# Optimization experiments

Hardware: AMD Instinct MI355X
Metric: run time of the kernel (lower is better)

The kernel has to match this reference:

```python
import jax, jax.numpy as jnp
import numpy as np

EMB = 256
N_HEADS = 8
N_LVLS = 4
N_POINTS = 4
HEAD_DIM = EMB // N_HEADS  # 32
D_FFN = 1024
SHAPES = [(100, 100), (50, 50), (25, 25), (13, 13)]
LEN = sum(h * w for h, w in SHAPES)  # 13294
B = 4


def setup_inputs() -> dict:
    key = jax.random.key(0)
    ks = jax.random.split(key, 20)
    rn = lambda k, s, sc=0.02: jax.random.normal(k, s, jnp.float32) * sc
    starts = np.cumsum([0] + [h * w for h, w in SHAPES])[:-1]
    return {
        'features': jax.random.normal(ks[0], (B, LEN, EMB), jnp.float32),
        'pos': jax.random.normal(ks[1], (B, LEN, EMB), jnp.float32),
        'reference_points': jax.random.uniform(ks[2], (B, LEN, N_LVLS, 2), jnp.float32),
        'spatial_shapes': jnp.array(SHAPES, jnp.int32),
        'lvl_start_idx': jnp.array(starts, jnp.int32),
        'W_off': rn(ks[3], (EMB, N_HEADS * N_LVLS * N_POINTS * 2)),
        'b_off': rn(ks[4], (N_HEADS * N_LVLS * N_POINTS * 2,), 0.5),
        'W_attn': rn(ks[5], (EMB, N_HEADS * N_LVLS * N_POINTS)),
        'b_attn': rn(ks[6], (N_HEADS * N_LVLS * N_POINTS,)),
        'W_val': rn(ks[7], (EMB, EMB)),
        'b_val': rn(ks[8], (EMB,)),
        'W_out': rn(ks[9], (EMB, EMB)),
        'b_out': rn(ks[10], (EMB,)),
        'ln1_g': jnp.ones((EMB,), jnp.float32),
        'ln1_b': jnp.zeros((EMB,), jnp.float32),
        'W1': rn(ks[11], (EMB, D_FFN)),
        'b1': rn(ks[12], (D_FFN,)),
        'W2': rn(ks[13], (D_FFN, EMB)),
        'b2': rn(ks[14], (EMB,)),
        'ln2_g': jnp.ones((EMB,), jnp.float32),
        'ln2_b': jnp.zeros((EMB,), jnp.float32),
    }


def _layer_norm(x, g, b, eps=1e-5):
    mu = jnp.mean(x, axis=-1, keepdims=True)
    var = jnp.mean(jnp.square(x - mu), axis=-1, keepdims=True)
    return (x - mu) * jax.lax.rsqrt(var + eps) * g + b


def _ms_deform_attn(q, features, reference_points, shapes, starts,
                    W_off, b_off, W_attn, b_attn, W_val, b_val, W_out, b_out):
    Bn, Lq, D = features.shape
    value = (features @ W_val + b_val).reshape(Bn, Lq, N_HEADS, HEAD_DIM)
    off = (q @ W_off + b_off).reshape(Bn, Lq, N_HEADS, N_LVLS, N_POINTS, 2)
    attn = (q @ W_attn + b_attn).reshape(Bn, Lq, N_HEADS, N_LVLS * N_POINTS)
    attn = jax.nn.softmax(attn, axis=-1).reshape(Bn, Lq, N_HEADS, N_LVLS, N_POINTS)
    # normalizer per level is (W, H) for (x, y)
    norm = jnp.array([[w, h] for h, w in shapes], jnp.float32)  # (L, 2)
    loc = reference_points[:, :, None, :, None, :] + off / norm[None, None, None, :, None, :]

    out = jnp.zeros((Bn, N_HEADS, Lq, HEAD_DIM), value.dtype)
    for l, (H_, W_) in enumerate(shapes):
        s = starts[l]
        val = value[:, s:s + H_ * W_].transpose(0, 2, 1, 3)  # (B, nH, HW, Dh)
        locl = loc[:, :, :, l]  # (B, Lq, nH, P, 2), in [0,1]
        # grid_sample align_corners=False convention
        x = locl[..., 0] * W_ - 0.5
        y = locl[..., 1] * H_ - 0.5
        x0 = jnp.floor(x); y0 = jnp.floor(y)
        wx = x - x0; wy = y - y0
        x0i = x0.astype(jnp.int32); y0i = y0.astype(jnp.int32)

        def corner(xi, yi, w):
            valid = (xi >= 0) & (xi < W_) & (yi >= 0) & (yi < H_)
            idx = jnp.clip(yi, 0, H_ - 1) * W_ + jnp.clip(xi, 0, W_ - 1)  # (B, Lq, nH, P)
            idx = idx.transpose(0, 2, 1, 3).reshape(Bn, N_HEADS, Lq * N_POINTS, 1)
            g = jnp.take_along_axis(val, idx, axis=2)  # (B, nH, Lq*P, Dh)
            wm = (w * valid.astype(w.dtype)).transpose(0, 2, 1, 3).reshape(Bn, N_HEADS, Lq * N_POINTS, 1)
            return g * wm

        samp = (corner(x0i, y0i, (1 - wx) * (1 - wy))
                + corner(x0i + 1, y0i, wx * (1 - wy))
                + corner(x0i, y0i + 1, (1 - wx) * wy)
                + corner(x0i + 1, y0i + 1, wx * wy))
        samp = samp.reshape(Bn, N_HEADS, Lq, N_POINTS, HEAD_DIM)
        aw = attn[:, :, :, l].transpose(0, 2, 1, 3)  # (B, nH, Lq, P)
        out = out + jnp.einsum('bhqpd,bhqp->bhqd', samp, aw)

    out = out.transpose(0, 2, 1, 3).reshape(Bn, Lq, D)
    return out @ W_out + b_out


def reference(features, pos, reference_points, spatial_shapes, lvl_start_idx,
              W_off, b_off, W_attn, b_attn, W_val, b_val, W_out, b_out,
              ln1_g, ln1_b, W1, b1, W2, b2, ln2_g, ln2_b):
    shapes = [tuple(int(v) for v in r) for r in np.asarray(spatial_shapes)]
    starts = [int(v) for v in np.asarray(lvl_start_idx)]
    q = features + pos
    attn_out = _ms_deform_attn(q, features, reference_points, shapes, starts,
                               W_off, b_off, W_attn, b_attn, W_val, b_val, W_out, b_out)
    x = _layer_norm(features + attn_out, ln1_g, ln1_b)  # dropout is identity in eval
    ffn = jax.nn.relu(x @ W1 + b1) @ W2 + b2
    x = _layer_norm(x + ffn, ln2_g, ln2_b)  # stochastic depth is identity in eval
    return x
```

## Files before the change

kernel.cpp:

```cpp
#include <hip/hip_runtime.h>
#include <stdint.h>

#define LEN_T 13294
#define M_TOK 53176

typedef unsigned short u16;
typedef __bf16 bf16x8 __attribute__((ext_vector_type(8)));
typedef float f32x4 __attribute__((ext_vector_type(4)));
typedef float f32x2 __attribute__((ext_vector_type(2)));
typedef uint32_t u32x4 __attribute__((ext_vector_type(4)));
typedef uint32_t u32x2 __attribute__((ext_vector_type(2)));

__device__ __forceinline__ u16 f2bf(float f) {
    union { float f; uint32_t u; } v; v.f = f;
    uint32_t r = v.u + 0x7fffu + ((v.u >> 16) & 1u);
    return (u16)(r >> 16);
}
__device__ __forceinline__ float bf2f(u16 s) {
    union { uint32_t u; float f; } v; v.u = ((uint32_t)s) << 16;
    return v.f;
}
__device__ __forceinline__ u16 f2h(float f) {
    union { _Float16 h; u16 u; } c; c.h = (_Float16)f; return c.u;
}
__device__ __forceinline__ float hlo(uint32_t u) {
    union { uint32_t u; _Float16 h[2]; } v; v.u = u; return (float)v.h[0];
}
__device__ __forceinline__ float hhi(uint32_t u) {
    union { uint32_t u; _Float16 h[2]; } v; v.u = u; return (float)v.h[1];
}

__device__ __forceinline__ void gload_lds16(const u16* g, u16* l) {
    __builtin_amdgcn_global_load_lds(
        (const __attribute__((address_space(1))) uint32_t*)(g),
        (__attribute__((address_space(3))) uint32_t*)(l), 16, 0, 0);
}

__global__ __launch_bounds__(256) void prep_qf(
    const float* __restrict__ feat, const float* __restrict__ pos,
    u16* __restrict__ qb, u16* __restrict__ fb, int n4)
{
    int i = blockIdx.x * blockDim.x + threadIdx.x;
    int stride = gridDim.x * blockDim.x;
    for (; i < n4; i += stride) {
        float4 f = ((const float4*)feat)[i];
        float4 p = ((const float4*)pos)[i];
        uint32_t q0 = (uint32_t)f2bf(f.x + p.x) | ((uint32_t)f2bf(f.y + p.y) << 16);
        uint32_t q1 = (uint32_t)f2bf(f.z + p.z) | ((uint32_t)f2bf(f.w + p.w) << 16);
        uint32_t f0 = (uint32_t)f2bf(f.x) | ((uint32_t)f2bf(f.y) << 16);
        uint32_t f1 = (uint32_t)f2bf(f.z) | ((uint32_t)f2bf(f.w) << 16);
        ((uint2*)qb)[i] = make_uint2(q0, q1);
        ((uint2*)fb)[i] = make_uint2(f0, f1);
    }
}

__global__ __launch_bounds__(256) void wtrans_all(
    const float* __restrict__ W_val, const float* __restrict__ W_off,
    const float* __restrict__ W_attn, const float* __restrict__ W_out,
    const float* __restrict__ W1, const float* __restrict__ W2,
    u16* __restrict__ Wt_val, u16* __restrict__ Wt_oa,
    u16* __restrict__ Wt_out, u16* __restrict__ W1f, u16* __restrict__ W2f)
{
    int gid = blockIdx.x * 256 + threadIdx.x;
    if (gid < 229376) {
        const float* W; u16* D; int K, N, off;
        if      (gid < 65536)  { W = W_val;  D = Wt_val;        K = 256; N = 256; off = gid; }
        else if (gid < 131072) { W = W_off;  D = Wt_oa;         K = 256; N = 256; off = gid - 65536; }
        else if (gid < 163840) { W = W_attn; D = Wt_oa + 65536; K = 256; N = 128; off = gid - 131072; }
        else                   { W = W_out;  D = Wt_out;        K = 256; N = 256; off = gid - 163840; }
        int n = off / K, k = off - n * K;
        D[off] = f2bf(W[(size_t)k * N + n]);
    } else if (gid < 491520) {
        int off = gid - 229376;
        int e = off & 7, lane = (off >> 3) & 63;
        int r = off >> 9;
        int ks = r & 7, ni = (r >> 3) & 1, c = r >> 4;
        int col = c * 32 + ni * 16 + (lane & 15);
        int k = ks * 32 + (lane >> 4) * 8 + e;
        W1f[off] = f2bf(W1[(size_t)k * 1024 + col]);
    } else if (gid < 753664) {
        int off = gid - 491520;
        int e = off & 7, lane = (off >> 3) & 63;
        int r = off >> 9;
        int col = (r & 15) * 16 + (lane & 15);
        int k = (r >> 4) * 32 + (lane >> 4) * 8 + e;
        W2f[off] = f2bf(W2[(size_t)k * 256 + col]);
    }
}

#define MODE_VAL 0
#define MODE_OFFATTN 1

template<int MODE>
__global__ __launch_bounds__(256, 3) void gemm128(
    const u16* __restrict__ A, const u16* __restrict__ Bt,
    int M, int K,
    const float* __restrict__ bias, const float* __restrict__ bias2,
    void* __restrict__ out0, void* __restrict__ out1)
{
    __shared__ u16 Al[128 * 64];
    __shared__ u16 Bl[128 * 64];
    const int tid = threadIdx.x;
    const int lane = tid & 63;
    const int w = tid >> 6;
    const int wr = w >> 1, wc = w & 1;
    const int m0 = blockIdx.x * 128;
    const int n0 = blockIdx.y * 128;
    const int l15 = lane & 15;
    const int kg = lane >> 4;
    const int srow = lane >> 3;
    const int scol = (lane & 7) * 8;

    f32x4 acc[4][4];
#pragma unroll
    for (int i = 0; i < 4; ++i)
#pragma unroll
        for (int j = 0; j < 4; ++j)
            acc[i][j] = (f32x4){0.f, 0.f, 0.f, 0.f};

    const int nk = K >> 6;
    for (int kc = 0; kc < nk; ++kc) {
        __syncthreads();
#pragma unroll
        for (int j = 0; j < 4; ++j) {
            int c = w * 4 + j;
            int arow = m0 + c * 8 + srow;
            arow = arow < M ? arow : M - 1;
            gload_lds16(A + (size_t)arow * K + (kc << 6) + scol, Al + c * 512);
            int brow = n0 + c * 8 + srow;
            gload_lds16(Bt + (size_t)brow * K + (kc << 6) + scol, Bl + c * 512);
        }
        __syncthreads();
#pragma unroll
        for (int ks = 0; ks < 2; ++ks) {
            bf16x8 af[4], bfr[4];
#pragma unroll
            for (int i = 0; i < 4; ++i) {
                af[i]  = *(const bf16x8*)(Al + (wr * 64 + i * 16 + l15) * 64 + ks * 32 + kg * 8);
                bfr[i] = *(const bf16x8*)(Bl + (wc * 64 + i * 16 + l15) * 64 + ks * 32 + kg * 8);
            }
#pragma unroll
            for (int mi = 0; mi < 4; ++mi)
#pragma unroll
                for (int ni = 0; ni < 4; ++ni)
                    acc[mi][ni] = __builtin_amdgcn_mfma_f32_16x16x32_bf16(
                        af[mi], bfr[ni], acc[mi][ni], 0, 0, 0);
        }
    }

#pragma unroll
    for (int mi = 0; mi < 4; ++mi) {
#pragma unroll
        for (int r = 0; r < 4; ++r) {
            int row = m0 + wr * 64 + mi * 16 + kg * 4 + r;
            if (row >= M) continue;
#pragma unroll
            for (int ni = 0; ni < 4; ++ni) {
                int col = n0 + wc * 64 + ni * 16 + l15;
                float v = acc[mi][ni][r];
                if (MODE == MODE_VAL) {
                    int bI = row / LEN_T;
                    int t = row - bI * LEN_T;
                    int hh = col >> 5, d = col & 31;
                    ((u16*)out0)[((size_t)(bI * 8 + hh) * LEN_T + t) * 32 + d] =
                        f2h(v + bias[col]);
                } else {
                    if (col < 256) {
                        ((u16*)out0)[((size_t)(col >> 5) * M_TOK + row) * 32 + (col & 31)] =
                            f2h(v + bias[col]);
                    } else {
                        int c = col - 256;
                        ((u16*)out1)[((size_t)(c >> 4) * M_TOK + row) * 16 + (c & 15)] =
                            f2h(v + bias2[c]);
                    }
                }
            }
        }
    }
}

template<int KSTEPS, int OUTF32>
__global__ __launch_bounds__(256, 3) void gemm_ln(
    const u16* __restrict__ A, const u16* __restrict__ Bt,
    const float* __restrict__ bias, const u16* __restrict__ res,
    const float* __restrict__ g, const float* __restrict__ bb,
    u16* __restrict__ outb, float* __restrict__ outf, int M)
{
    __shared__ char ldsraw[40960];
    u16* Al = (u16*)ldsraw;
    u16* Bl = (u16*)(ldsraw + 8192);
    u16* dumpb = (u16*)ldsraw;
    const int tid = threadIdx.x;
    const int lane = tid & 63;
    const int w = tid >> 6;
    const int l15 = lane & 15;
    const int kg = lane >> 4;
    const int srow = lane >> 3;
    const int scol = (lane & 7) * 8;
    const int m0 = blockIdx.x * 64;
    const int K = KSTEPS * 64;

    f32x4 acc[4][4];
#pragma unroll
    for (int i = 0; i < 4; ++i)
#pragma unroll
        for (int j = 0; j < 4; ++j)
            acc[i][j] = (f32x4){0.f, 0.f, 0.f, 0.f};

    for (int kc = 0; kc < KSTEPS; ++kc) {
        __syncthreads();
#pragma unroll
        for (int j = 0; j < 2; ++j) {
            int c = w * 2 + j;
            int arow = m0 + c * 8 + srow;
            arow = arow < M ? arow : M - 1;
            gload_lds16(A + (size_t)arow * K + (kc << 6) + scol, Al + c * 512);
        }
#pragma unroll
        for (int j = 0; j < 8; ++j) {
            int c = w * 8 + j;
            int brow = c * 8 + srow;
            gload_lds16(Bt + (size_t)brow * K + (kc << 6) + scol, Bl + c * 512);
        }
        __syncthreads();
#pragma unroll
        for (int ks = 0; ks < 2; ++ks) {
            bf16x8 af[4], bfr[4];
#pragma unroll
            for (int i = 0; i < 4; ++i) {
                af[i]  = *(const bf16x8*)(Al + (i * 16 + l15) * 64 + ks * 32 + kg * 8);
                bfr[i] = *(const bf16x8*)(Bl + (w * 64 + i * 16 + l15) * 64 + ks * 32 + kg * 8);
            }
#pragma unroll
            for (int mi = 0; mi < 4; ++mi)
#pragma unroll
                for (int ni = 0; ni < 4; ++ni)
                    acc[mi][ni] = __builtin_amdgcn_mfma_f32_16x16x32_bf16(
                        af[mi], bfr[ni], acc[mi][ni], 0, 0, 0);
        }
    }

    __syncthreads();
#pragma unroll
    for (int mi = 0; mi < 4; ++mi) {
#pragma unroll
        for (int r = 0; r < 4; ++r) {
            int rr = mi * 16 + kg * 4 + r;
            int gr = m0 + rr; gr = gr < M ? gr : M - 1;
#pragma unroll
            for (int ni = 0; ni < 4; ++ni) {
                int col = w * 64 + ni * 16 + l15;
                dumpb[rr * 264 + col] = f2bf(acc[mi][ni][r] + bias[col] +
                                             bf2f(res[(size_t)gr * 256 + col]));
            }
        }
    }
    __syncthreads();

    float4 gv = *(const float4*)(g + lane * 4);
    float4 bv = *(const float4*)(bb + lane * 4);
#pragma unroll
    for (int i = 0; i < 16; ++i) {
        int rr = w * 16 + i;
        uint2 raw = *(const uint2*)(dumpb + rr * 264 + lane * 4);
        float x0 = bf2f((u16)(raw.x & 0xffff)), x1 = bf2f((u16)(raw.x >> 16));
        float x2 = bf2f((u16)(raw.y & 0xffff)), x3 = bf2f((u16)(raw.y >> 16));
        float s1 = x0 + x1 + x2 + x3;
        float s2 = x0*x0 + x1*x1 + x2*x2 + x3*x3;
#pragma unroll
        for (int o = 1; o < 64; o <<= 1) {
            s1 += __shfl_xor(s1, o);
            s2 += __shfl_xor(s2, o);
        }
        float mu = s1 * (1.0f / 256.0f);
        float var = s2 * (1.0f / 256.0f) - mu * mu;
        float rs = rsqrtf(var + 1e-5f);
        float o0 = (x0 - mu) * rs * gv.x + bv.x;
        float o1 = (x1 - mu) * rs * gv.y + bv.y;
        float o2 = (x2 - mu) * rs * gv.z + bv.z;
        float o3 = (x3 - mu) * rs * gv.w + bv.w;
        int grow = m0 + rr;
        if (grow < M) {
            if (OUTF32) {
                *(float4*)(outf + (size_t)grow * 256 + lane * 4) =
                    make_float4(o0, o1, o2, o3);
            } else {
                uint32_t u0 = (uint32_t)f2bf(o0) | ((uint32_t)f2bf(o1) << 16);
                uint32_t u1 = (uint32_t)f2bf(o2) | ((uint32_t)f2bf(o3) << 16);
                *(uint2*)(outb + (size_t)grow * 256 + lane * 4) = make_uint2(u0, u1);
            }
        }
    }
}

__global__ __launch_bounds__(256, 3) void ffn_fused(
    const u16* __restrict__ A, const u16* __restrict__ W1f, const u16* __restrict__ W2f,
    const float* __restrict__ b1, const float* __restrict__ b2,
    const float* __restrict__ g, const float* __restrict__ bb,
    float* __restrict__ outf, int M)
{
    __shared__ char lds[51200];
    u16* Axl = (u16*)lds;
    u16* ht  = (u16*)(lds + 33792);
    u16* dumpb = (u16*)lds;
    const int tid = threadIdx.x;
    const int lane = tid & 63;
    const int w = tid >> 6;
    const int l15 = lane & 15;
    const int kg = lane >> 4;
    const int m0 = blockIdx.x * 64;

#pragma unroll
    for (int i = 0; i < 8; ++i) {
        int linear = i * 256 + tid;
        int row = linear >> 5;
        int gcol = (linear & 31) * 8;
        int grow = m0 + row; grow = grow < M ? grow : M - 1;
        uint4 v = *(const uint4*)(A + (size_t)grow * 256 + gcol);
        *(uint4*)(Axl + row * 264 + gcol) = v;
    }
    __syncthreads();

    f32x4 acc[4][4];
#pragma unroll
    for (int i = 0; i < 4; ++i)
#pragma unroll
        for (int j = 0; j < 4; ++j)
            acc[i][j] = (f32x4){0.f, 0.f, 0.f, 0.f};
    f32x4 acc2[4][2];

#define ZERO_ACC2() \
    _Pragma("unroll") for (int i = 0; i < 4; ++i) { \
        acc2[i][0] = (f32x4){0.f,0.f,0.f,0.f}; acc2[i][1] = (f32x4){0.f,0.f,0.f,0.f}; }

#define FFN1_CHUNK(HC) { \
    _Pragma("unroll") for (int ks = 0; ks < 8; ++ks) { \
        bf16x8 af[4], bw[2]; \
        _Pragma("unroll") for (int ni = 0; ni < 2; ++ni) \
            bw[ni] = *(const bf16x8*)(W1f + ((size_t)(((((HC) * 4 + w) * 2 + ni) * 8 + ks)) << 9) + lane * 8); \
        _Pragma("unroll") for (int mi = 0; mi < 4; ++mi) \
            af[mi] = *(const bf16x8*)(Axl + (mi * 16 + l15) * 264 + ks * 32 + kg * 8); \
        _Pragma("unroll") for (int mi = 0; mi < 4; ++mi) \
            _Pragma("unroll") for (int ni = 0; ni < 2; ++ni) \
                acc2[mi][ni] = __builtin_amdgcn_mfma_f32_16x16x32_bf16(af[mi], bw[ni], acc2[mi][ni], 0, 0, 0); \
    } }

#define FFN2_CHUNK(HC) { \
    _Pragma("unroll") for (int ks2 = 0; ks2 < 4; ++ks2) { \
        bf16x8 ah[4], bw2[4]; \
        _Pragma("unroll") for (int ni = 0; ni < 4; ++ni) \
            bw2[ni] = *(const bf16x8*)(W2f + ((size_t)((((HC) * 4 + ks2) * 16 + w * 4 + ni)) << 9) + lane * 8); \
        _Pragma("unroll") for (int mi = 0; mi < 4; ++mi) \
            ah[mi] = *(const bf16x8*)(ht + (mi * 16 + l15) * 136 + ks2 * 32 + kg * 8); \
        _Pragma("unroll") for (int mi = 0; mi < 4; ++mi) \
            _Pragma("unroll") for (int ni = 0; ni < 4; ++ni) \
                acc[mi][ni] = __builtin_amdgcn_mfma_f32_16x16x32_bf16(ah[mi], bw2[ni], acc[mi][ni], 0, 0, 0); \
    } }

#define HT_WRITE(HC) { \
    _Pragma("unroll") for (int mi = 0; mi < 4; ++mi) \
        _Pragma("unroll") for (int ni = 0; ni < 2; ++ni) \
            _Pragma("unroll") for (int r = 0; r < 4; ++r) { \
                int rr = mi * 16 + kg * 4 + r; \
                int cl = w * 32 + ni * 16 + l15; \
                float hv = acc2[mi][ni][r] + b1[(HC) * 128 + cl]; \
                ht[rr * 136 + cl] = f2bf(hv > 0.f ? hv : 0.f); \
            } }

    ZERO_ACC2();
    FFN1_CHUNK(0);
    for (int hc = 0; hc < 8; ++hc) {
        __syncthreads();
        HT_WRITE(hc);
        __syncthreads();
        FFN2_CHUNK(hc);
        if (hc < 7) { ZERO_ACC2(); FFN1_CHUNK(hc + 1); }
    }

#pragma unroll
    for (int mi = 0; mi < 4; ++mi) {
#pragma unroll
        for (int r = 0; r < 4; ++r) {
            int rr = mi * 16 + kg * 4 + r;
#pragma unroll
            for (int ni = 0; ni < 4; ++ni) {
                int col = w * 64 + ni * 16 + l15;
                float v = acc[mi][ni][r] + b2[col] + bf2f(Axl[rr * 264 + col]);
                dumpb[rr * 264 + col] = f2bf(v);
            }
        }
    }
    __syncthreads();

    float4 gv = *(const float4*)(g + lane * 4);
    float4 bv = *(const float4*)(bb + lane * 4);
#pragma unroll
    for (int i = 0; i < 16; ++i) {
        int rr = w * 16 + i;
        uint2 raw = *(const uint2*)(dumpb + rr * 264 + lane * 4);
        float x0 = bf2f((u16)(raw.x & 0xffff)), x1 = bf2f((u16)(raw.x >> 16));
        float x2 = bf2f((u16)(raw.y & 0xffff)), x3 = bf2f((u16)(raw.y >> 16));
        float s1 = x0 + x1 + x2 + x3;
        float s2 = x0*x0 + x1*x1 + x2*x2 + x3*x3;
#pragma unroll
        for (int o = 1; o < 64; o <<= 1) {
            s1 += __shfl_xor(s1, o);
            s2 += __shfl_xor(s2, o);
        }
        float mu = s1 * (1.0f / 256.0f);
        float var = s2 * (1.0f / 256.0f) - mu * mu;
        float rs = rsqrtf(var + 1e-5f);
        float o0 = (x0 - mu) * rs * gv.x + bv.x;
        float o1 = (x1 - mu) * rs * gv.y + bv.y;
        float o2 = (x2 - mu) * rs * gv.z + bv.z;
        float o3 = (x3 - mu) * rs * gv.w + bv.w;
        int grow = m0 + rr;
        if (grow < M) {
            *(float4*)(outf + (size_t)grow * 256 + lane * 4) =
                make_float4(o0, o1, o2, o3);
        }
    }
}

__device__ __forceinline__ void acc8h(u32x4 v, float w, float* acc) {
    acc[0] = fmaf(hlo(v.x), w, acc[0]);
    acc[1] = fmaf(hhi(v.x), w, acc[1]);
    acc[2] = fmaf(hlo(v.y), w, acc[2]);
    acc[3] = fmaf(hhi(v.y), w, acc[3]);
    acc[4] = fmaf(hlo(v.z), w, acc[4]);
    acc[5] = fmaf(hhi(v.z), w, acc[5]);
    acc[6] = fmaf(hlo(v.w), w, acc[6]);
    acc[7] = fmaf(hhi(v.w), w, acc[7]);
}

__global__ __launch_bounds__(256, 4) void sample_kernel(
    const u16* __restrict__ offt, const u16* __restrict__ attnt,
    const u16* __restrict__ value, const float* __restrict__ refp,
    u16* __restrict__ samp)
{
    int bid = blockIdx.x;
    int lb  = (bid & 7) * 832 + (bid >> 3);
    int bh  = lb / 208;
    int tblk = lb - bh * 208;
    int pr  = threadIdx.x >> 2;
    int dq  = threadIdx.x & 3;
    int tok = tblk * 64 + pr;
    if (tok >= LEN_T) return;
    int b = bh >> 3, h = bh & 7;
    int lane = threadIdx.x & 63;
    size_t row = (size_t)b * LEN_T + tok;

    int W_    = dq == 0 ? 100 : dq == 1 ? 50 : dq == 2 ? 25 : 13;
    float Wf   = dq == 0 ? 100.f : dq == 1 ? 50.f : dq == 2 ? 25.f : 13.f;
    float invW = dq == 0 ? 0.01f : dq == 1 ? 0.02f : dq == 2 ? 0.04f : (1.0f / 13.0f);

    u32x2 av = __builtin_nontemporal_load(
        (const u32x2*)(attnt + ((size_t)h * M_TOK + row) * 16 + dq * 4));
    float e0 = hlo(av.x), e1 = hhi(av.x), e2 = hlo(av.y), e3 = hhi(av.y);
    float m = fmaxf(fmaxf(e0, e1), fmaxf(e2, e3));
    m = fmaxf(m, __shfl_xor(m, 1));
    m = fmaxf(m, __shfl_xor(m, 2));
    e0 = __expf(e0 - m); e1 = __expf(e1 - m);
    e2 = __expf(e2 - m); e3 = __expf(e3 - m);
    float s = e0 + e1 + e2 + e3;
    s += __shfl_xor(s, 1);
    s += __shfl_xor(s, 2);
    float inv = 1.0f / s;
    float awp[4] = {e0 * inv, e1 * inv, e2 * inv, e3 * inv};

    f32x2 rv = __builtin_nontemporal_load((const f32x2*)(refp + row * 8 + dq * 2));
    float rx = rv.x, ry = rv.y;
    u32x4 ov = __builtin_nontemporal_load(
        (const u32x4*)(offt + ((size_t)h * M_TOK + row) * 32 + dq * 8));
    float dxs[4] = {hlo(ov.x), hlo(ov.y), hlo(ov.z), hlo(ov.w)};
    float dys[4] = {hhi(ov.x), hhi(ov.y), hhi(ov.z), hhi(ov.w)};

    float wts[16]; int offs[16];
#pragma unroll
    for (int p = 0; p < 4; ++p) {
        float x = fmaf(fmaf(dxs[p], invW, rx), Wf, -0.5f);
        float y = fmaf(fmaf(dys[p], invW, ry), Wf, -0.5f);
        float x0f = floorf(x), y0f = floorf(y);
        int x0 = (int)x0f, y0 = (int)y0f;
        int x1 = x0 + 1, y1 = y0 + 1;
        float wx = x - x0f, wy = y - y0f;
        float vx0 = ((unsigned)x0 < (unsigned)W_) ? 1.f : 0.f;
        float vx1 = ((unsigned)x1 < (unsigned)W_) ? 1.f : 0.f;
        float vy0 = ((unsigned)y0 < (unsigned)W_) ? 1.f : 0.f;
        float vy1 = ((unsigned)y1 < (unsigned)W_) ? 1.f : 0.f;
        int cx0 = min(max(x0, 0), W_ - 1);
        int cx1 = min(max(x1, 0), W_ - 1);
        int cy0 = min(max(y0, 0), W_ - 1);
        int cy1 = min(max(y1, 0), W_ - 1);
        float a = awp[p];
        wts[p*4+0] = (1.f - wx) * (1.f - wy) * a * vx0 * vy0;
        wts[p*4+1] = wx * (1.f - wy) * a * vx1 * vy0;
        wts[p*4+2] = (1.f - wx) * wy * a * vx0 * vy1;
        wts[p*4+3] = wx * wy * a * vx1 * vy1;
        offs[p*4+0] = (cy0 * W_ + cx0) * 32;
        offs[p*4+1] = (cy0 * W_ + cx1) * 32;
        offs[p*4+2] = (cy1 * W_ + cx0) * 32;
        offs[p*4+3] = (cy1 * W_ + cx1) * 32;
    }

    float acc[8];
#pragma unroll
    for (int d = 0; d < 8; ++d) acc[d] = 0.f;
    const int qbase = lane & ~3;

#pragma unroll
    for (int l2 = 0; l2 < 4; ++l2) {
        const int SL2 = (l2 == 0) ? 0 : (l2 == 1) ? 10000 : (l2 == 2) ? 12500 : 13125;
        const u16* vb = value + ((size_t)bh * LEN_T + SL2) * 32 + dq * 8;
        const int src = qbase + l2;
#pragma unroll
        for (int c2 = 0; c2 < 2; ++c2) {
            float w8[8]; int o8[8];
#pragma unroll
            for (int i = 0; i < 8; ++i) {
                w8[i] = __shfl(wts[c2*8 + i], src);
                o8[i] = __shfl(offs[c2*8 + i], src);
            }
            u32x4 vv[8];
#pragma unroll
            for (int i = 0; i < 8; ++i)
                vv[i] = *(const u32x4*)(vb + o8[i]);
#pragma unroll
            for (int i = 0; i < 8; ++i)
                acc8h(vv[i], w8[i], acc);
        }
    }
    u32x4 uo;
    uo.x = (uint32_t)f2bf(acc[0]) | ((uint32_t)f2bf(acc[1]) << 16);
    uo.y = (uint32_t)f2bf(acc[2]) | ((uint32_t)f2bf(acc[3]) << 16);
    uo.z = (uint32_t)f2bf(acc[4]) | ((uint32_t)f2bf(acc[5]) << 16);
    uo.w = (uint32_t)f2bf(acc[6]) | ((uint32_t)f2bf(acc[7]) << 16);
    __builtin_nontemporal_store(uo, (u32x4*)(samp + row * 256 + h * 32 + dq * 8));
}

extern "C" void kernel_launch(void* const* d_in, const int* in_sizes, int n_in,
                              void* d_out, int out_size, void* d_ws, size_t ws_size,
                              hipStream_t stream)
{
    const float* features = (const float*)d_in[0];
    const float* pos      = (const float*)d_in[1];
    const float* refp     = (const float*)d_in[2];
    const float* W_off  = (const float*)d_in[5];
    const float* b_off  = (const float*)d_in[6];
    const float* W_attn = (const float*)d_in[7];
    const float* b_attn = (const float*)d_in[8];
    const float* W_val  = (const float*)d_in[9];
    const float* b_val  = (const float*)d_in[10];
    const float* W_out  = (const float*)d_in[11];
    const float* b_out  = (const float*)d_in[12];
    const float* ln1_g  = (const float*)d_in[13];
    const float* ln1_b  = (const float*)d_in[14];
    const float* W1     = (const float*)d_in[15];
    const float* b1     = (const float*)d_in[16];
    const float* W2     = (const float*)d_in[17];
    const float* b2     = (const float*)d_in[18];
    const float* ln2_g  = (const float*)d_in[19];
    const float* ln2_b  = (const float*)d_in[20];
    float* out = (float*)d_out;

    char* ws = (char*)d_ws;
    size_t o = 0;
    auto alloc = [&](size_t bytes) { char* p = ws + o; o += (bytes + 255) & ~(size_t)255; return p; };
    u16* Wt_val = (u16*)alloc((size_t)256 * 256 * 2);
    u16* Wt_oa  = (u16*)alloc((size_t)384 * 256 * 2);
    u16* Wt_out = (u16*)alloc((size_t)256 * 256 * 2);
    u16* W1f    = (u16*)alloc((size_t)1024 * 256 * 2);
    u16* W2f    = (u16*)alloc((size_t)256 * 1024 * 2);
    u16* qb     = (u16*)alloc((size_t)M_TOK * 256 * 2);
    u16* fb     = (u16*)alloc((size_t)M_TOK * 256 * 2);
    char* big   = alloc((size_t)M_TOK * 1024 * 2);
    u16* value  = (u16*)big;
    u16* offt   = (u16*)(big + (size_t)M_TOK * 256 * 2);
    u16* attnt  = (u16*)(big + (size_t)M_TOK * 256 * 2 * 2);
    u16* samp = qb;
    u16* xb   = qb;

    dim3 blk(256);
    const int mb  = (M_TOK + 127) / 128;
    const int mb64 = (M_TOK + 63) / 64;

    prep_qf<<<2048, blk, 0, stream>>>(features, pos, qb, fb, M_TOK * 256 / 4);
    wtrans_all<<<2944, blk, 0, stream>>>(W_val, W_off, W_attn, W_out, W1, W2,
                                         Wt_val, Wt_oa, Wt_out, W1f, W2f);

    gemm128<MODE_VAL><<<dim3(mb, 2), blk, 0, stream>>>(
        fb, Wt_val, M_TOK, 256, b_val, nullptr, value, nullptr);
    gemm128<MODE_OFFATTN><<<dim3(mb, 3), blk, 0, stream>>>(
        qb, Wt_oa, M_TOK, 256, b_off, b_attn, offt, attnt);

    sample_kernel<<<6656, blk, 0, stream>>>(offt, attnt, value, refp, samp);

    gemm_ln<4, 0><<<mb64, blk, 0, stream>>>(
        samp, Wt_out, b_out, fb, ln1_g, ln1_b, xb, nullptr, M_TOK);

    ffn_fused<<<mb64, blk, 0, stream>>>(
        xb, W1f, W2f, b1, b2, ln2_g, ln2_b, out, M_TOK);
}
```

Baseline: 336.2 us.

## Restructure fused FFN so each wave owns 16 rows end-to-end without block syncs

The fused FFN kernel now gives each wave its own 16 token rows. Each wave keeps its input A fragments in registers, computes all 128 hidden columns per chunk and all 256 output columns, and uses a private LDS slice for the hidden tile, so the block-wide __syncthreads are gone. W1 is repacked so each chunk's columns are contiguous for this per-wave layout. LayerNorm is done directly from the accumulators with 16-lane shuffles, and the residual is read from global memory. The trade-off is higher register pressure (launch bounds drop to 2 blocks), fewer ways to reuse each weight fragment across rows, so weight global/L2 traffic per token roughly quadruples, and the output stores are scalar and strided.

Result: slower. 504.2 us (+50.0%).

```diff
diff --git a/kernel.cpp b/kernel.cpp
--- a/kernel.cpp
+++ b/kernel.cpp
@@ -74,8 +74,8 @@
         int off = gid - 229376;
         int e = off & 7, lane = (off >> 3) & 63;
         int r = off >> 9;
-        int ks = r & 7, ni = (r >> 3) & 1, c = r >> 4;
-        int col = c * 32 + ni * 16 + (lane & 15);
+        int ks = r & 7, ni = (r >> 3) & 7, hc = r >> 6;
+        int col = hc * 128 + ni * 16 + (lane & 15);
         int k = ks * 32 + (lane >> 4) * 8 + e;
         W1f[off] = f2bf(W1[(size_t)k * 1024 + col]);
     } else if (gid < 753664) {
@@ -293,131 +293,104 @@
     }
 }
 
-__global__ __launch_bounds__(256, 3) void ffn_fused(
-    const u16* __restrict__ A, const u16* __restrict__ W1f, const u16* __restrict__ W2f,
+__global__ __launch_bounds__(256, 2) void ffn_fused(
+    const u16* __restrict__ xb, const u16* __restrict__ W1f, const u16* __restrict__ W2f,
     const float* __restrict__ b1, const float* __restrict__ b2,
     const float* __restrict__ g, const float* __restrict__ bb,
     float* __restrict__ outf, int M)
 {
-    __shared__ char lds[51200];
-    u16* Axl = (u16*)lds;
-    u16* ht  = (u16*)(lds + 33792);
-    u16* dumpb = (u16*)lds;
-    const int tid = threadIdx.x;
-    const int lane = tid & 63;
-    const int w = tid >> 6;
+    __shared__ u16 ht_all[4 * 16 * 136];
+    const int lane = threadIdx.x & 63;
+    const int w = threadIdx.x >> 6;
     const int l15 = lane & 15;
     const int kg = lane >> 4;
-    const int m0 = blockIdx.x * 64;
-
-#pragma unroll
-    for (int i = 0; i < 8; ++i) {
-        int linear = i * 256 + tid;
-        int row = linear >> 5;
-        int gcol = (linear & 31) * 8;
-        int grow = m0 + row; grow = grow < M ? grow : M - 1;
-        uint4 v = *(const uint4*)(A + (size_t)grow * 256 + gcol);
-        *(uint4*)(Axl + row * 264 + gcol) = v;
-    }
-    __syncthreads();
-
-    f32x4 acc[4][4];
-#pragma unroll
-    for (int i = 0; i < 4; ++i)
-#pragma unroll
-        for (int j = 0; j < 4; ++j)
-            acc[i][j] = (f32x4){0.f, 0.f, 0.f, 0.f};
-    f32x4 acc2[4][2];
-
-#define ZERO_ACC2() \
-    _Pragma("unroll") for (int i = 0; i < 4; ++i) { \
-        acc2[i][0] = (f32x4){0.f,0.f,0.f,0.f}; acc2[i][1] = (f32x4){0.f,0.f,0.f,0.f}; }
-
-#define FFN1_CHUNK(HC) { \
-    _Pragma("unroll") for (int ks = 0; ks < 8; ++ks) { \
-        bf16x8 af[4], bw[2]; \
-        _Pragma("unroll") for (int ni = 0; ni < 2; ++ni) \
-            bw[ni] = *(const bf16x8*)(W1f + ((size_t)(((((HC) * 4 + w) * 2 + ni) * 8 + ks)) << 9) + lane * 8); \
-        _Pragma("unroll") for (int mi = 0; mi < 4; ++mi) \
-            af[mi] = *(const bf16x8*)(Axl + (mi * 16 + l15) * 264 + ks * 32 + kg * 8); \
-        _Pragma("unroll") for (int mi = 0; mi < 4; ++mi) \
-            _Pragma("unroll") for (int ni = 0; ni < 2; ++ni) \
-                acc2[mi][ni] = __builtin_amdgcn_mfma_f32_16x16x32_bf16(af[mi], bw[ni], acc2[mi][ni], 0, 0, 0); \
-    } }
-
-#define FFN2_CHUNK(HC) { \
-    _Pragma("unroll") for (int ks2 = 0; ks2 < 4; ++ks2) { \
-        bf16x8 ah[4], bw2[4]; \
-        _Pragma("unroll") for (int ni = 0; ni < 4; ++ni) \
-            bw2[ni] = *(const bf16x8*)(W2f + ((size_t)((((HC) * 4 + ks2) * 16 + w * 4 + ni)) << 9) + lane * 8); \
-        _Pragma("unroll") for (int mi = 0; mi < 4; ++mi) \
-            ah[mi] = *(const bf16x8*)(ht + (mi * 16 + l15) * 136 + ks2 * 32 + kg * 8); \
-        _Pragma("unroll") for (int mi = 0; mi < 4; ++mi) \
-            _Pragma("unroll") for (int ni = 0; ni < 4; ++ni) \
-                acc[mi][ni] = __builtin_amdgcn_mfma_f32_16x16x32_bf16(ah[mi], bw2[ni], acc[mi][ni], 0, 0, 0); \
-    } }
-
-#define HT_WRITE(HC) { \
-    _Pragma("unroll") for (int mi = 0; mi < 4; ++mi) \
-        _Pragma("unroll") for (int ni = 0; ni < 2; ++ni) \
-            _Pragma("unroll") for (int r = 0; r < 4; ++r) { \
-                int rr = mi * 16 + kg * 4 + r; \
-                int cl = w * 32 + ni * 16 + l15; \
-                float hv = acc2[mi][ni][r] + b1[(HC) * 128 + cl]; \
-                ht[rr * 136 + cl] = f2bf(hv > 0.f ? hv : 0.f); \
-            } }
-
-    ZERO_ACC2();
-    FFN1_CHUNK(0);
+    const int m0w = blockIdx.x * 64 + w * 16;
+    u16* ht = ht_all + w * (16 * 136);
+
+    int arow = m0w + l15; arow = arow < M ? arow : M - 1;
+    const u16* xrow = xb + (size_t)arow * 256 + kg * 8;
+    bf16x8 af[8];
+#pragma unroll
+    for (int ks = 0; ks < 8; ++ks)
+        af[ks] = *(const bf16x8*)(xrow + ks * 32);
+
+    f32x4 acc[16];
+#pragma unroll
+    for (int i = 0; i < 16; ++i) acc[i] = (f32x4){0.f, 0.f, 0.f, 0.f};
+
     for (int hc = 0; hc < 8; ++hc) {
-        __syncthreads();
-        HT_WRITE(hc);
-        __syncthreads();
-        FFN2_CHUNK(hc);
-        if (hc < 7) { ZERO_ACC2(); FFN1_CHUNK(hc + 1); }
-    }
-
-#pragma unroll
-    for (int mi = 0; mi < 4; ++mi) {
-#pragma unroll
-        for (int r = 0; r < 4; ++r) {
-            int rr = mi * 16 + kg * 4 + r;
-#pragma unroll
-            for (int ni = 0; ni < 4; ++ni) {
-                int col = w * 64 + ni * 16 + l15;
-                float v = acc[mi][ni][r] + b2[col] + bf2f(Axl[rr * 264 + col]);
-                dumpb[rr * 264 + col] = f2bf(v);
-            }
-        }
-    }
-    __syncthreads();
-
-    float4 gv = *(const float4*)(g + lane * 4);
-    float4 bv = *(const float4*)(bb + lane * 4);
-#pragma unroll
-    for (int i = 0; i < 16; ++i) {
-        int rr = w * 16 + i;
-        uint2 raw = *(const uint2*)(dumpb + rr * 264 + lane * 4);
-        float x0 = bf2f((u16)(raw.x & 0xffff)), x1 = bf2f((u16)(raw.x >> 16));
-        float x2 = bf2f((u16)(raw.y & 0xffff)), x3 = bf2f((u16)(raw.y >> 16));
-        float s1 = x0 + x1 + x2 + x3;
-        float s2 = x0*x0 + x1*x1 + x2*x2 + x3*x3;
-#pragma unroll
-        for (int o = 1; o < 64; o <<= 1) {
+        f32x4 acc2[8];
+#pragma unroll
+        for (int i = 0; i < 8; ++i) acc2[i] = (f32x4){0.f, 0.f, 0.f, 0.f};
+#pragma unroll
+        for (int ks = 0; ks < 8; ++ks) {
+            bf16x8 bw[8];
+#pragma unroll
+            for (int ni = 0; ni < 8; ++ni)
+                bw[ni] = *(const bf16x8*)(W1f +
+                    ((size_t)(((hc * 8 + ni) * 8 + ks)) << 9) + lane * 8);
+#pragma unroll
+            for (int ni = 0; ni < 8; ++ni)
+                acc2[ni] = __builtin_amdgcn_mfma_f32_16x16x32_bf16(
+                    af[ks], bw[ni], acc2[ni], 0, 0, 0);
+        }
+#pragma unroll
+        for (int ni = 0; ni < 8; ++ni) {
+#pragma unroll
+            for (int r = 0; r < 4; ++r) {
+                float hv = acc2[ni][r] + b1[hc * 128 + ni * 16 + l15];
+                ht[(kg * 4 + r) * 136 + ni * 16 + l15] = f2bf(hv > 0.f ? hv : 0.f);
+            }
+        }
+#pragma unroll
+        for (int ks2 = 0; ks2 < 4; ++ks2) {
+            bf16x8 ah = *(const bf16x8*)(ht + l15 * 136 + ks2 * 32 + kg * 8);
+            bf16x8 bw2[16];
+#pragma unroll
+            for (int ni = 0; ni < 16; ++ni)
+                bw2[ni] = *(const bf16x8*)(W2f +
+                    ((size_t)(((hc * 4 + ks2) * 16 + ni)) << 9) + lane * 8);
+#pragma unroll
+            for (int ni = 0; ni < 16; ++ni)
+                acc[ni] = __builtin_amdgcn_mfma_f32_16x16x32_bf16(
+                    ah, bw2[ni], acc[ni], 0, 0, 0);
+        }
+    }
+
+    float b2c[16], gc[16], bc[16];
+#pragma unroll
+    for (int ni = 0; ni < 16; ++ni) {
+        b2c[ni] = b2[ni * 16 + l15];
+        gc[ni]  = g[ni * 16 + l15];
+        bc[ni]  = bb[ni * 16 + l15];
+    }
+#pragma unroll
+    for (int r = 0; r < 4; ++r) {
+        int row = m0w + kg * 4 + r;
+        int rowc = row < M ? row : M - 1;
+        float vals[16];
+        float s1 = 0.f, s2 = 0.f;
+#pragma unroll
+        for (int ni = 0; ni < 16; ++ni) {
+            float v = acc[ni][r] + b2c[ni] +
+                      bf2f(xb[(size_t)rowc * 256 + ni * 16 + l15]);
+            vals[ni] = v;
+            s1 += v;
+            s2 += v * v;
+        }
+#pragma unroll
+        for (int o = 1; o < 16; o <<= 1) {
             s1 += __shfl_xor(s1, o);
             s2 += __shfl_xor(s2, o);
         }
         float mu = s1 * (1.0f / 256.0f);
         float var = s2 * (1.0f / 256.0f) - mu * mu;
         float rs = rsqrtf(var + 1e-5f);
-        float o0 = (x0 - mu) * rs * gv.x + bv.x;
-        float o1 = (x1 - mu) * rs * gv.y + bv.y;
-        float o2 = (x2 - mu) * rs * gv.z + bv.z;
-        float o3 = (x3 - mu) * rs * gv.w + bv.w;
-        int grow = m0 + rr;
-        if (grow < M) {
-            *(float4*)(outf + (size_t)grow * 256 + lane * 4) =
-                make_float4(o0, o1, o2, o3);
+        if (row < M) {
+#pragma unroll
+            for (int ni = 0; ni < 16; ++ni)
+                outf[(size_t)row * 256 + ni * 16 + l15] =
+                    (vals[ni] - mu) * rs * gc[ni] + bc[ni];
         }
     }
 }
```
